# Kernel optimization log

Measured on AMD Instinct MI355X. Metric: run time of the kernel, lower is better.

Reference implementation:

```python
import jax, jax.numpy as jnp
import numpy as np

B, C, H, W_SP = 16, 128, 28, 28
F, KS, STRIDE, PAD = 128, 3, 1, 1
CHUNK = 4      # filters per chunk for the L1 reduction (limits intermediate size)
EPS = 1e-12


def setup_inputs() -> dict:
    key = jax.random.key(0)
    kx, kw = jax.random.split(key)
    x = jax.random.normal(kx, (B, C, H, W_SP), dtype=jnp.float32)
    # kaiming_normal_: std = sqrt(2 / fan_in), fan_in = C*KS*KS
    std = float(np.sqrt(2.0 / (C * KS * KS)))
    W = jax.random.normal(kw, (F, C, KS, KS), dtype=jnp.float32) * std
    return {"x": x, "W": W}


def _patches(x):
    # im2col: [B, C*KS*KS, h_out, w_out], feature order (c, kh, kw) like torch unfold
    p = jax.lax.conv_general_dilated_patches(
        x, (KS, KS), (STRIDE, STRIDE), [(PAD, PAD), (PAD, PAD)],
        dimension_numbers=('NCHW', 'OIHW', 'NCHW'))
    b, k, ho, wo = p.shape
    return p.reshape(b, k, ho * wo), ho, wo


def reference(x, W):
    P, ho, wo = _patches(x)          # [B, K, L]
    Wc = W.reshape(F, -1)            # [F, K]
    K = Wc.shape[1]

    # Forward value: out = -cdist_L1(W, X_col) = -sum_k |W[f,k] - P[b,k,l]|
    # computed in filter chunks to avoid the full [F, K, B*L] diff tensor.
    Wch = Wc.reshape(F // CHUNK, CHUNK, K)
    def chunk_fn(wc):                # wc: [CHUNK, K]
        return jnp.sum(jnp.abs(wc[None, :, :, None] - P[:, None, :, :]), axis=2)  # [B, CHUNK, L]
    neg_l1 = -jax.lax.map(chunk_fn, Wch)                     # [F//CHUNK, B, CHUNK, L]
    neg_l1 = jnp.transpose(neg_l1, (1, 0, 2, 3)).reshape(P.shape[0], F, -1)  # [B, F, L]

    # Gradient path in original (straight-through): -cdist_L2, via GEMM decomposition.
    d2 = (jnp.sum(Wc * Wc, axis=1)[None, :, None]
          + jnp.sum(P * P, axis=1)[:, None, :]
          - 2.0 * jnp.einsum('fk,bkl->bfl', Wc, P))
    neg_l2 = -jnp.sqrt(jnp.maximum(d2, EPS))

    # value = -L1, gradient flows through -L2 (out.data = out_2.data in torch)
    out = neg_l2 + jax.lax.stop_gradient(neg_l1 - neg_l2)    # [B, F, L]
    return out.reshape(P.shape[0], F, ho, wo)
```

## Files before the change

### kernel.cpp

```cpp
#include <hip/hip_runtime.h>


#define B_    16
#define C_    128
#define HH    28
#define WW    28
#define F_    128
#define L_    (HH * WW)
#define K_    (C_ * 9)
#define M_    (B_ * L_)
#define TM    64
#define BC    4
#define KC    (BC * 9)
#define KP    (KC / 2)
#define SLAB  (B_ * F_ * L_)
#define NMT   (M_ / TM)
#define QS    4096.0f
#define QB    32768.5f

__device__ __forceinline__ unsigned sad16(unsigned a, unsigned b, unsigned c) {
    asm("v_sad_u16 %0, %1, %2, %0" : "+v"(c) : "v"(a), "v"(b));
    return c;
}

__global__ __launch_bounds__(256, 4)
void adder2d_main(const float* __restrict__ x, const float* __restrict__ Wg,
                  float* __restrict__ dst, int nch, int direct) {
    __shared__ __align__(16) unsigned Plq[KP][TM];
    __shared__ __align__(16) unsigned Wlq[KP][F_];

    const int t    = threadIdx.x;
    const int lane = t & 63;
    const int w    = t >> 6;
    const int tx   = lane & 7;
    const int ty   = lane >> 3;
    const int fw   = 32 * w;
    const int mt   = blockIdx.x, sp = blockIdx.z;
    const int c0   = sp * nch * BC;

    const int m  = mt * TM + lane;
    const int b  = m / L_;
    const int l  = m - b * L_;
    const int ho = l / WW, wo = l - ho * WW;
    int   toff[9];
    float sc[9];
    #pragma unroll
    for (int r = 0; r < 9; ++r) {
        const int dy = r / 3 - 1;
        const int dx = r - (r / 3) * 3 - 1;
        const bool ok = ((unsigned)(ho + dy) < (unsigned)HH) &&
                        ((unsigned)(wo + dx) < (unsigned)WW);
        toff[r] = ok ? (dy * WW + dx) : 0;
        sc[r]   = ok ? QS : 0.0f;
    }
    const float* xb = x + (size_t)b * (C_ * L_) + l;

    const int cp = w >> 1;
    const int r0 = (w & 1) ? 5 : 0;
    const int fW = t >> 1;
    const int pW = t & 1;
    const float* wbase = Wg + (size_t)fW * K_;

    unsigned acc[8][4];
    #pragma unroll
    for (int i = 0; i < 8; ++i)
        #pragma unroll
        for (int j = 0; j < 4; ++j) acc[i][j] = 0u;

    float ppre[10];
    float wpre[18];

    auto loadP = [&](int c8) {
        const float* x1 = xb + (size_t)(c8 + cp) * L_;
        const float* x2 = x1 + 2 * L_;
        #pragma unroll
        for (int i = 0; i < 5; ++i) {
            const int r  = r0 + i;
            const int rr = (r > 8) ? 8 : r;
            ppre[i]     = x1[toff[rr]];
            ppre[5 + i] = x2[toff[rr]];
        }
    };
    auto loadW = [&](int c8) {
        const float* w1 = wbase + (size_t)(c8 + pW) * 9;
        #pragma unroll
        for (int i = 0; i < 9; ++i) {
            wpre[i]     = w1[i];
            wpre[9 + i] = w1[18 + i];
        }
    };

    loadP(c0);
    loadW(c0);

    #pragma unroll 1
    for (int ch = 0; ch < nch; ++ch) {
        #pragma unroll
        for (int i = 0; i < 5; ++i) {
            const int r = r0 + i;
            if (r <= 8) {
                const unsigned qlo = (unsigned)__builtin_fmaf(ppre[i],     sc[r], QB);
                const unsigned qhi = (unsigned)__builtin_fmaf(ppre[5 + i], sc[r], QB);
                Plq[cp * 9 + r][lane] = (qlo & 0xffffu) | (qhi << 16);
            }
        }
        #pragma unroll
        for (int i = 0; i < 9; ++i) {
            const unsigned qlo = (unsigned)__builtin_fmaf(wpre[i],     QS, QB);
            const unsigned qhi = (unsigned)__builtin_fmaf(wpre[9 + i], QS, QB);
            Wlq[pW * 9 + i][fW] = (qlo & 0xffffu) | (qhi << 16);
        }
        if (ch + 1 < nch) {
            loadP(c0 + (ch + 1) * BC);
            loadW(c0 + (ch + 1) * BC);
        }
        asm volatile("s_waitcnt lgkmcnt(0)" ::: "memory");
        __builtin_amdgcn_s_barrier();
        asm volatile("" ::: "memory");
        __builtin_amdgcn_sched_barrier(0);
        #pragma unroll 6
        for (int kp = 0; kp < KP; ++kp) {
            const uint4 pA = *(const uint4*)&Plq[kp][tx * 8];
            const uint4 pB = *(const uint4*)&Plq[kp][tx * 8 + 4];
            const uint4 wA = *(const uint4*)&Wlq[kp][fw + ty * 4];
            const unsigned pm[8] = {pA.x, pA.y, pA.z, pA.w,
                                    pB.x, pB.y, pB.z, pB.w};
            const unsigned wn[4] = {wA.x, wA.y, wA.z, wA.w};
            #pragma unroll
            for (int i = 0; i < 8; ++i)
                #pragma unroll
                for (int j = 0; j < 4; ++j)
                    acc[i][j] = sad16(pm[i], wn[j], acc[i][j]);
        }
        if (ch + 1 < nch) {
            asm volatile("" ::: "memory");
            __builtin_amdgcn_sched_barrier(0);
            __builtin_amdgcn_s_barrier();
            asm volatile("" ::: "memory");
        }
    }

    const int mb = mt * TM + tx * 8;
    const int bI = mb / L_;
    const int lb = mb - bI * L_;
    float* slab = direct ? dst : dst + (size_t)sp * SLAB;
    const float qs = (direct ? -1.0f : 1.0f) / QS;
    #pragma unroll
    for (int j = 0; j < 4; ++j) {
        const int f = fw + ty * 4 + j;
        float* o = &slab[(size_t)(bI * F_ + f) * L_ + lb];
        *(float4*)o       = make_float4(qs * (float)acc[0][j], qs * (float)acc[1][j],
                                        qs * (float)acc[2][j], qs * (float)acc[3][j]);
        *(float4*)(o + 4) = make_float4(qs * (float)acc[4][j], qs * (float)acc[5][j],
                                        qs * (float)acc[6][j], qs * (float)acc[7][j]);
    }
}

__global__ __launch_bounds__(256)
void adder2d_combine(const float* __restrict__ ws, float* __restrict__ out,
                     int nslab) {
    const int i = blockIdx.x * 256 + threadIdx.x;
    float4 r = make_float4(0.0f, 0.0f, 0.0f, 0.0f);
    for (int s = 0; s < nslab; ++s) {
        const float4 p = ((const float4*)(ws + (size_t)s * SLAB))[i];
        r.x += p.x; r.y += p.y; r.z += p.z; r.w += p.w;
    }
    ((float4*)out)[i] = make_float4(-r.x, -r.y, -r.z, -r.w);
}

extern "C" void kernel_launch(void* const* d_in, const int* in_sizes, int n_in,
                              void* d_out, int out_size, void* d_ws, size_t ws_size,
                              hipStream_t stream) {
    const float* x = (const float*)d_in[0];
    const float* W = (const float*)d_in[1];
    float* out = (float*)d_out;
    float* ws  = (float*)d_ws;

    int split = 0;
    if (ws_size >= (size_t)8 * SLAB * sizeof(float))      split = 8;
    else if (ws_size >= (size_t)4 * SLAB * sizeof(float)) split = 4;

    if (split) {
        dim3 grid(NMT, 1, split);
        adder2d_main<<<grid, 256, 0, stream>>>(x, W, ws, (C_ / BC) / split, 0);
        adder2d_combine<<<SLAB / 4 / 256, 256, 0, stream>>>(ws, out, split);
    } else {
        dim3 grid(NMT, 1, 1);
        adder2d_main<<<grid, 256, 0, stream>>>(x, W, out, C_ / BC, 1);
    }
}
```

Measured before the change: 112.8 us.

## Fuse split-K slab reduction into main kernel via last-block atomic counter

Removes the separate combine kernel. Each block now bumps a per-M-tile atomic counter after writing its partial slab, and the last block for that tile sums all slabs and writes the negated output. This saves a kernel launch and lets the reduction overlap with other blocks still computing. In exchange it adds a memset launch for the counters, thread fences, and a serialized reduction tail inside the last-arriving blocks.

Measured after the change: 421.3 us. 3.73x slower.

```diff
diff --git a/kernel.cpp b/kernel.cpp
--- a/kernel.cpp
+++ b/kernel.cpp
@@ -25,9 +25,11 @@
 
 __global__ __launch_bounds__(256, 4)
 void adder2d_main(const float* __restrict__ x, const float* __restrict__ Wg,
-                  float* __restrict__ dst, int nch, int direct) {
+                  float* __restrict__ slabs, float* __restrict__ out,
+                  unsigned* __restrict__ cnt, int nch, int nsp, int direct) {
     __shared__ __align__(16) unsigned Plq[KP][TM];
     __shared__ __align__(16) unsigned Wlq[KP][F_];
+    __shared__ unsigned redFlag;
 
     const int t    = threadIdx.x;
     const int lane = t & 63;
@@ -143,29 +145,39 @@
     const int mb = mt * TM + tx * 8;
     const int bI = mb / L_;
     const int lb = mb - bI * L_;
-    float* slab = direct ? dst : dst + (size_t)sp * SLAB;
+    float* dstp = direct ? out : slabs + (size_t)sp * SLAB;
     const float qs = (direct ? -1.0f : 1.0f) / QS;
     #pragma unroll
     for (int j = 0; j < 4; ++j) {
         const int f = fw + ty * 4 + j;
-        float* o = &slab[(size_t)(bI * F_ + f) * L_ + lb];
+        float* o = &dstp[(size_t)(bI * F_ + f) * L_ + lb];
         *(float4*)o       = make_float4(qs * (float)acc[0][j], qs * (float)acc[1][j],
                                         qs * (float)acc[2][j], qs * (float)acc[3][j]);
         *(float4*)(o + 4) = make_float4(qs * (float)acc[4][j], qs * (float)acc[5][j],
                                         qs * (float)acc[6][j], qs * (float)acc[7][j]);
     }
-}
-
-__global__ __launch_bounds__(256)
-void adder2d_combine(const float* __restrict__ ws, float* __restrict__ out,
-                     int nslab) {
-    const int i = blockIdx.x * 256 + threadIdx.x;
-    float4 r = make_float4(0.0f, 0.0f, 0.0f, 0.0f);
-    for (int s = 0; s < nslab; ++s) {
-        const float4 p = ((const float4*)(ws + (size_t)s * SLAB))[i];
-        r.x += p.x; r.y += p.y; r.z += p.z; r.w += p.w;
-    }
-    ((float4*)out)[i] = make_float4(-r.x, -r.y, -r.z, -r.w);
+
+    if (direct) return;
+
+    __threadfence();
+    if (t == 0) {
+        const unsigned old = atomicAdd(&cnt[mt], 1u);
+        redFlag = (old == (unsigned)(nsp - 1)) ? 1u : 0u;
+    }
+    __syncthreads();
+    if (redFlag) {
+        __threadfence();
+        const size_t base0 = (size_t)b * (F_ * L_) + l;
+        #pragma unroll 4
+        for (int i = 0; i < 32; ++i) {
+            const int f = (t >> 6) + 4 * i;
+            const size_t off = base0 + (size_t)f * L_;
+            float s = 0.0f;
+            for (int s2 = 0; s2 < nsp; ++s2)
+                s += slabs[(size_t)s2 * SLAB + off];
+            out[off] = -s;
+        }
+    }
 }
 
 extern "C" void kernel_launch(void* const* d_in, const int* in_sizes, int n_in,
@@ -176,16 +188,19 @@
     float* out = (float*)d_out;
     float* ws  = (float*)d_ws;
 
-    int split = 0;
-    if (ws_size >= (size_t)8 * SLAB * sizeof(float))      split = 8;
-    else if (ws_size >= (size_t)4 * SLAB * sizeof(float)) split = 4;
-
-    if (split) {
-        dim3 grid(NMT, 1, split);
-        adder2d_main<<<grid, 256, 0, stream>>>(x, W, ws, (C_ / BC) / split, 0);
-        adder2d_combine<<<SLAB / 4 / 256, 256, 0, stream>>>(ws, out, split);
+    int nsp = 0;
+    if (ws_size >= (size_t)8 * SLAB * sizeof(float) + 1024)      nsp = 8;
+    else if (ws_size >= (size_t)4 * SLAB * sizeof(float) + 1024) nsp = 4;
+
+    if (nsp) {
+        unsigned* cnt = (unsigned*)(ws + (size_t)nsp * SLAB);
+        hipMemsetAsync(cnt, 0, NMT * sizeof(unsigned), stream);
+        dim3 grid(NMT, 1, nsp);
+        adder2d_main<<<grid, 256, 0, stream>>>(x, W, ws, out, cnt,
+                                               (C_ / BC) / nsp, nsp, 0);
     } else {
         dim3 grid(NMT, 1, 1);
-        adder2d_main<<<grid, 256, 0, stream>>>(x, W, out, C_ / BC, 1);
+        adder2d_main<<<grid, 256, 0, stream>>>(x, W, nullptr, out, nullptr,
+                                               C_ / BC, 1, 1);
     }
 }
```

## Double channel chunk per barrier, load weights directly, fix split-K at four

Applied to the files above, without the earlier changes.

Raises the channel chunk per LDS stage from 4 to 8, which halves the number of barrier rounds and doubles the inner SAD loop length per stage. Each wave now loads all 9 taps for its channel pair. Weights are read from global memory inside the loop instead of being register-prefetched, which removes register pressure but exposes weight-load latency before the barrier. The split-K factor is fixed at 4 instead of preferring 8, which cuts combine traffic but reduces grid parallelism.

Result: no change. 114.3 us (+1.3%).

```diff
diff --git a/kernel.cpp b/kernel.cpp
--- a/kernel.cpp
+++ b/kernel.cpp
@@ -10,7 +10,7 @@
 #define K_    (C_ * 9)
 #define M_    (B_ * L_)
 #define TM    64
-#define BC    4
+#define BC    8
 #define KC    (BC * 9)
 #define KP    (KC / 2)
 #define SLAB  (B_ * F_ * L_)
@@ -55,8 +55,7 @@
     }
     const float* xb = x + (size_t)b * (C_ * L_) + l;
 
-    const int cp = w >> 1;
-    const int r0 = (w & 1) ? 5 : 0;
+    const int pb = (w & 1) + 4 * (w >> 1);
     const int fW = t >> 1;
     const int pW = t & 1;
     const float* wbase = Wg + (size_t)fW * K_;
@@ -67,53 +66,39 @@
         #pragma unroll
         for (int j = 0; j < 4; ++j) acc[i][j] = 0u;
 
-    float ppre[10];
-    float wpre[18];
-
+    float ppre[18];
     auto loadP = [&](int c8) {
-        const float* x1 = xb + (size_t)(c8 + cp) * L_;
+        const float* x1 = xb + (size_t)(c8 + pb) * L_;
         const float* x2 = x1 + 2 * L_;
         #pragma unroll
-        for (int i = 0; i < 5; ++i) {
-            const int r  = r0 + i;
-            const int rr = (r > 8) ? 8 : r;
-            ppre[i]     = x1[toff[rr]];
-            ppre[5 + i] = x2[toff[rr]];
-        }
-    };
-    auto loadW = [&](int c8) {
-        const float* w1 = wbase + (size_t)(c8 + pW) * 9;
-        #pragma unroll
-        for (int i = 0; i < 9; ++i) {
-            wpre[i]     = w1[i];
-            wpre[9 + i] = w1[18 + i];
+        for (int r = 0; r < 9; ++r) {
+            ppre[r]     = x1[toff[r]];
+            ppre[9 + r] = x2[toff[r]];
         }
     };
 
     loadP(c0);
-    loadW(c0);
 
     #pragma unroll 1
     for (int ch = 0; ch < nch; ++ch) {
+        const int c8 = c0 + ch * BC;
         #pragma unroll
-        for (int i = 0; i < 5; ++i) {
-            const int r = r0 + i;
-            if (r <= 8) {
-                const unsigned qlo = (unsigned)__builtin_fmaf(ppre[i],     sc[r], QB);
-                const unsigned qhi = (unsigned)__builtin_fmaf(ppre[5 + i], sc[r], QB);
-                Plq[cp * 9 + r][lane] = (qlo & 0xffffu) | (qhi << 16);
+        for (int r = 0; r < 9; ++r) {
+            const unsigned qlo = (unsigned)__builtin_fmaf(ppre[r],     sc[r], QB);
+            const unsigned qhi = (unsigned)__builtin_fmaf(ppre[9 + r], sc[r], QB);
+            Plq[w * 9 + r][lane] = (qlo & 0xffffu) | (qhi << 16);
+        }
+        #pragma unroll
+        for (int s = 0; s < 2; ++s) {
+            const float* w1 = wbase + (size_t)(c8 + pW + 4 * s) * 9;
+            #pragma unroll
+            for (int i = 0; i < 9; ++i) {
+                const unsigned qlo = (unsigned)__builtin_fmaf(w1[i],      QS, QB);
+                const unsigned qhi = (unsigned)__builtin_fmaf(w1[i + 18], QS, QB);
+                Wlq[(pW + 2 * s) * 9 + i][fW] = (qlo & 0xffffu) | (qhi << 16);
             }
         }
-        #pragma unroll
-        for (int i = 0; i < 9; ++i) {
-            const unsigned qlo = (unsigned)__builtin_fmaf(wpre[i],     QS, QB);
-            const unsigned qhi = (unsigned)__builtin_fmaf(wpre[9 + i], QS, QB);
-            Wlq[pW * 9 + i][fW] = (qlo & 0xffffu) | (qhi << 16);
-        }
-        if (ch + 1 < nch) {
-            loadP(c0 + (ch + 1) * BC);
-            loadW(c0 + (ch + 1) * BC);
-        }
+        if (ch + 1 < nch) loadP(c8 + BC);
         asm volatile("s_waitcnt lgkmcnt(0)" ::: "memory");
         __builtin_amdgcn_s_barrier();
         asm volatile("" ::: "memory");
@@ -176,14 +161,11 @@
     float* out = (float*)d_out;
     float* ws  = (float*)d_ws;
 
-    int split = 0;
-    if (ws_size >= (size_t)8 * SLAB * sizeof(float))      split = 8;
-    else if (ws_size >= (size_t)4 * SLAB * sizeof(float)) split = 4;
-
-    if (split) {
-        dim3 grid(NMT, 1, split);
-        adder2d_main<<<grid, 256, 0, stream>>>(x, W, ws, (C_ / BC) / split, 0);
-        adder2d_combine<<<SLAB / 4 / 256, 256, 0, stream>>>(ws, out, split);
+    const int nsp = 4;
+    if (ws_size >= (size_t)nsp * SLAB * sizeof(float)) {
+        dim3 grid(NMT, 1, nsp);
+        adder2d_main<<<grid, 256, 0, stream>>>(x, W, ws, (C_ / BC) / nsp, 0);
+        adder2d_combine<<<SLAB / 4 / 256, 256, 0, stream>>>(ws, out, nsp);
     } else {
         dim3 grid(NMT, 1, 1);
         adder2d_main<<<grid, 256, 0, stream>>>(x, W, out, C_ / BC, 1);
```

## Enlarge per-thread SAD tile to 8x8 with intra-block K split and LDS reduction

Applied to the files above, without the earlier changes.

Each thread now accumulates an 8x8 tile instead of 8x4, so fewer LDS reads are needed per SAD instruction. The four waves split into two filter halves and two K halves, and the K halves are combined through an LDS reduction before only half the waves write output. The split-K factor across blocks is fixed at 4 instead of preferring 8, which halves the partial slabs the combine kernel must read. The cost is more accumulator registers (occupancy hint lowered from 4 to 3), extra barriers for the reduction, and less grid parallelism.

After: 120.4 us. +6.7%, slower.

```diff
diff --git a/kernel.cpp b/kernel.cpp
--- a/kernel.cpp
+++ b/kernel.cpp
@@ -13,28 +13,34 @@
 #define BC    4
 #define KC    (BC * 9)
 #define KP    (KC / 2)
+#define NSP   4
+#define NCH   ((C_ / BC) / NSP)
 #define SLAB  (B_ * F_ * L_)
 #define NMT   (M_ / TM)
 #define QS    4096.0f
 #define QB    32768.5f
 
+#define SMEMW (KP * TM + KP * F_)
+
 __device__ __forceinline__ unsigned sad16(unsigned a, unsigned b, unsigned c) {
     asm("v_sad_u16 %0, %1, %2, %0" : "+v"(c) : "v"(a), "v"(b));
     return c;
 }
 
-__global__ __launch_bounds__(256, 4)
+__global__ __launch_bounds__(256, 3)
 void adder2d_main(const float* __restrict__ x, const float* __restrict__ Wg,
                   float* __restrict__ dst, int nch, int direct) {
-    __shared__ __align__(16) unsigned Plq[KP][TM];
-    __shared__ __align__(16) unsigned Wlq[KP][F_];
+    __shared__ __align__(16) unsigned smem[SMEMW];
+    #define PLQ(kp, m) smem[(kp) * TM + (m)]
+    #define WLQ(kp, f) smem[KP * TM + (kp) * F_ + (f)]
 
     const int t    = threadIdx.x;
     const int lane = t & 63;
     const int w    = t >> 6;
     const int tx   = lane & 7;
     const int ty   = lane >> 3;
-    const int fw   = 32 * w;
+    const int fh   = w & 1;
+    const int kh   = w >> 1;
     const int mt   = blockIdx.x, sp = blockIdx.z;
     const int c0   = sp * nch * BC;
 
@@ -61,11 +67,11 @@
     const int pW = t & 1;
     const float* wbase = Wg + (size_t)fW * K_;
 
-    unsigned acc[8][4];
+    unsigned acc[8][8];
     #pragma unroll
     for (int i = 0; i < 8; ++i)
         #pragma unroll
-        for (int j = 0; j < 4; ++j) acc[i][j] = 0u;
+        for (int j = 0; j < 8; ++j) acc[i][j] = 0u;
 
     float ppre[10];
     float wpre[18];
@@ -101,14 +107,14 @@
             if (r <= 8) {
                 const unsigned qlo = (unsigned)__builtin_fmaf(ppre[i],     sc[r], QB);
                 const unsigned qhi = (unsigned)__builtin_fmaf(ppre[5 + i], sc[r], QB);
-                Plq[cp * 9 + r][lane] = (qlo & 0xffffu) | (qhi << 16);
+                PLQ(cp * 9 + r, lane) = (qlo & 0xffffu) | (qhi << 16);
             }
         }
         #pragma unroll
         for (int i = 0; i < 9; ++i) {
             const unsigned qlo = (unsigned)__builtin_fmaf(wpre[i],     QS, QB);
             const unsigned qhi = (unsigned)__builtin_fmaf(wpre[9 + i], QS, QB);
-            Wlq[pW * 9 + i][fW] = (qlo & 0xffffu) | (qhi << 16);
+            WLQ(pW * 9 + i, fW) = (qlo & 0xffffu) | (qhi << 16);
         }
         if (ch + 1 < nch) {
             loadP(c0 + (ch + 1) * BC);
@@ -118,18 +124,21 @@
         __builtin_amdgcn_s_barrier();
         asm volatile("" ::: "memory");
         __builtin_amdgcn_sched_barrier(0);
-        #pragma unroll 6
-        for (int kp = 0; kp < KP; ++kp) {
-            const uint4 pA = *(const uint4*)&Plq[kp][tx * 8];
-            const uint4 pB = *(const uint4*)&Plq[kp][tx * 8 + 4];
-            const uint4 wA = *(const uint4*)&Wlq[kp][fw + ty * 4];
+        #pragma unroll
+        for (int kk = 0; kk < 9; ++kk) {
+            const int kp = kh * 9 + kk;
+            const uint4 pA = *(const uint4*)&PLQ(kp, tx * 8);
+            const uint4 pB = *(const uint4*)&PLQ(kp, tx * 8 + 4);
+            const uint4 wA = *(const uint4*)&WLQ(kp, fh * 64 + ty * 8);
+            const uint4 wB = *(const uint4*)&WLQ(kp, fh * 64 + ty * 8 + 4);
             const unsigned pm[8] = {pA.x, pA.y, pA.z, pA.w,
                                     pB.x, pB.y, pB.z, pB.w};
-            const unsigned wn[4] = {wA.x, wA.y, wA.z, wA.w};
+            const unsigned wn[8] = {wA.x, wA.y, wA.z, wA.w,
+                                    wB.x, wB.y, wB.z, wB.w};
             #pragma unroll
             for (int i = 0; i < 8; ++i)
                 #pragma unroll
-                for (int j = 0; j < 4; ++j)
+                for (int j = 0; j < 8; ++j)
                     acc[i][j] = sad16(pm[i], wn[j], acc[i][j]);
         }
         if (ch + 1 < nch) {
@@ -140,20 +149,70 @@
         }
     }
 
-    const int mb = mt * TM + tx * 8;
-    const int bI = mb / L_;
-    const int lb = mb - bI * L_;
-    float* slab = direct ? dst : dst + (size_t)sp * SLAB;
-    const float qs = (direct ? -1.0f : 1.0f) / QS;
+    asm volatile("" ::: "memory");
+    __builtin_amdgcn_sched_barrier(0);
+    __builtin_amdgcn_s_barrier();
+    asm volatile("" ::: "memory");
+    unsigned* red = smem;
+    const int slot = (fh * 64 + lane) * 16;
     #pragma unroll
-    for (int j = 0; j < 4; ++j) {
-        const int f = fw + ty * 4 + j;
-        float* o = &slab[(size_t)(bI * F_ + f) * L_ + lb];
-        *(float4*)o       = make_float4(qs * (float)acc[0][j], qs * (float)acc[1][j],
-                                        qs * (float)acc[2][j], qs * (float)acc[3][j]);
-        *(float4*)(o + 4) = make_float4(qs * (float)acc[4][j], qs * (float)acc[5][j],
-                                        qs * (float)acc[6][j], qs * (float)acc[7][j]);
-    }
+    for (int p = 0; p < 4; ++p) {
+        if (kh == 1) {
+            #pragma unroll
+            for (int q = 0; q < 4; ++q) {
+                const int v = p * 16 + q * 4;
+                uint4 val;
+                val.x = acc[(v + 0) >> 3][(v + 0) & 7];
+                val.y = acc[(v + 1) >> 3][(v + 1) & 7];
+                val.z = acc[(v + 2) >> 3][(v + 2) & 7];
+                val.w = acc[(v + 3) >> 3][(v + 3) & 7];
+                *(uint4*)&red[slot + q * 4] = val;
+            }
+        }
+        asm volatile("s_waitcnt lgkmcnt(0)" ::: "memory");
+        __builtin_amdgcn_s_barrier();
+        asm volatile("" ::: "memory");
+        if (kh == 0) {
+            #pragma unroll
+            for (int q = 0; q < 4; ++q) {
+                const int v = p * 16 + q * 4;
+                const uint4 r2 = *(const uint4*)&red[slot + q * 4];
+                acc[(v + 0) >> 3][(v + 0) & 7] += r2.x;
+                acc[(v + 1) >> 3][(v + 1) & 7] += r2.y;
+                acc[(v + 2) >> 3][(v + 2) & 7] += r2.z;
+                acc[(v + 3) >> 3][(v + 3) & 7] += r2.w;
+            }
+        }
+        if (p < 3) {
+            asm volatile("" ::: "memory");
+            __builtin_amdgcn_sched_barrier(0);
+            __builtin_amdgcn_s_barrier();
+            asm volatile("" ::: "memory");
+        }
+    }
+
+    if (kh == 0) {
+        const int mb = mt * TM + tx * 8;
+        const int bI = mb / L_;
+        const int lb = mb - bI * L_;
+        float* slab = direct ? dst : dst + (size_t)sp * SLAB;
+        const float qs = (direct ? -1.0f : 1.0f) / QS;
+        #pragma unroll
+        for (int j = 0; j < 8; ++j) {
+            const int f = fh * 64 + ty * 8 + j;
+            float* o = &slab[(size_t)(bI * F_ + f) * L_ + lb];
+            *(float4*)o       = make_float4(qs * (float)acc[0][j],
+                                            qs * (float)acc[1][j],
+                                            qs * (float)acc[2][j],
+                                            qs * (float)acc[3][j]);
+            *(float4*)(o + 4) = make_float4(qs * (float)acc[4][j],
+                                            qs * (float)acc[5][j],
+                                            qs * (float)acc[6][j],
+                                            qs * (float)acc[7][j]);
+        }
+    }
+    #undef PLQ
+    #undef WLQ
 }
 
 __global__ __launch_bounds__(256)
@@ -176,14 +235,10 @@
     float* out = (float*)d_out;
     float* ws  = (float*)d_ws;
 
-    int split = 0;
-    if (ws_size >= (size_t)8 * SLAB * sizeof(float))      split = 8;
-    else if (ws_size >= (size_t)4 * SLAB * sizeof(float)) split = 4;
-
-    if (split) {
-        dim3 grid(NMT, 1, split);
-        adder2d_main<<<grid, 256, 0, stream>>>(x, W, ws, (C_ / BC) / split, 0);
-        adder2d_combine<<<SLAB / 4 / 256, 256, 0, stream>>>(ws, out, split);
+    if (ws_size >= (size_t)NSP * SLAB * sizeof(float)) {
+        dim3 grid(NMT, 1, NSP);
+        adder2d_main<<<grid, 256, 0, stream>>>(x, W, ws, NCH, 0);
+        adder2d_combine<<<SLAB / 4 / 256, 256, 0, stream>>>(ws, out, NSP);
     } else {
         dim3 grid(NMT, 1, 1);
         adder2d_main<<<grid, 256, 0, stream>>>(x, W, out, C_ / BC, 1);
```
